# Performance work log

Hardware: AMD Instinct MI355X
Metric: run time of the kernel (lower is better)

The kernel has to match this reference:

```python
import jax, jax.numpy as jnp
import numpy as np

HIDDEN = 512


def lstm_layer(x, W_ih, W_hh, b_ih, b_hh):
    """Single LSTM layer, batch_first. x: [B,T,I] -> hs: [B,T,H].
    PyTorch gate order: i, f, g, o."""
    B = x.shape[0]
    H = W_hh.shape[1]
    # Input contribution for all timesteps at once: [B,T,4H]
    pre = jnp.einsum('bti,gi->btg', x, W_ih) + b_ih + b_hh

    def step(carry, p_t):
        h, c = carry                      # [B,H] each
        gates = p_t + h @ W_hh.T          # [B,4H]
        i, f, g, o = jnp.split(gates, 4, axis=-1)
        i = jax.nn.sigmoid(i)
        f = jax.nn.sigmoid(f)
        g = jnp.tanh(g)
        o = jax.nn.sigmoid(o)
        c = f * c + i * g
        h = o * jnp.tanh(c)
        return (h, c), h

    init = (jnp.zeros((B, H), x.dtype), jnp.zeros((B, H), x.dtype))
    _, hs = jax.lax.scan(step, init, jnp.swapaxes(pre, 0, 1))  # hs: [T,B,H]
    return jnp.swapaxes(hs, 0, 1)


def setup_inputs() -> dict:
    key = jax.random.key(0)
    ks = jax.random.split(key, 11)
    B, T, I, H, C = 128, 512, 64, HIDDEN, 3
    s = 1.0 / np.sqrt(H)  # PyTorch LSTM init scale
    return {
        'state': jax.random.normal(ks[0], (B, T, I), dtype=jnp.float32),
        'W_ih0': jax.random.normal(ks[1], (4 * H, I), dtype=jnp.float32) * s,
        'W_hh0': jax.random.normal(ks[2], (4 * H, H), dtype=jnp.float32) * s,
        'b_ih0': jax.random.normal(ks[3], (4 * H,), dtype=jnp.float32) * s,
        'b_hh0': jax.random.normal(ks[4], (4 * H,), dtype=jnp.float32) * s,
        'W_ih1': jax.random.normal(ks[5], (4 * H, H), dtype=jnp.float32) * s,
        'W_hh1': jax.random.normal(ks[6], (4 * H, H), dtype=jnp.float32) * s,
        'b_ih1': jax.random.normal(ks[7], (4 * H,), dtype=jnp.float32) * s,
        'b_hh1': jax.random.normal(ks[8], (4 * H,), dtype=jnp.float32) * s,
        'W_out': jax.random.normal(ks[9], (C, H), dtype=jnp.float32) * s,
        'b_out': jax.random.normal(ks[10], (C,), dtype=jnp.float32) * s,
    }


def reference(state, W_ih0, W_hh0, b_ih0, b_hh0,
              W_ih1, W_hh1, b_ih1, b_hh1, W_out, b_out):
    # 2-layer LSTM (zero initial h/c, eval mode so inter-layer dropout is inert)
    h1 = lstm_layer(state, W_ih0, W_hh0, b_ih0, b_hh0)  # [B,T,H]
    h2 = lstm_layer(h1, W_ih1, W_hh1, b_ih1, b_hh1)     # [B,T,H]
    last = h2[:, -1, :]                                  # [B,H]
    return last @ W_out.T + b_out                        # [B,nClasses]
```

## Files before the change

kernel.cpp:

```cpp
#include <hip/hip_runtime.h>
#include <hip/hip_bf16.h>
#include <cstddef>

#define B_ 128
#define T_ 512
#define I_ 64
#define H_ 512

typedef __attribute__((ext_vector_type(8))) short short8v;
typedef __attribute__((ext_vector_type(4))) float f32x4;

__device__ __forceinline__ unsigned short f2bf(float f) {
  union { float f; unsigned u; } v; v.f = f;
  unsigned r = (v.u + 0x7FFFu + ((v.u >> 16) & 1u)) >> 16;
  return (unsigned short)r;
}
__device__ __forceinline__ float sigm(float x) { return 1.0f / (1.0f + __expf(-x)); }
__device__ __forceinline__ float tanh_(float x) {
  float t = __expf(2.0f * x);
  return 1.0f - 2.0f / (t + 1.0f);
}

template<int PASS>
__global__ __launch_bounds__(256, 1)
void lstm_pass(const float* __restrict__ Wih, const float* __restrict__ Whh,
               const float* __restrict__ bih, const float* __restrict__ bhh,
               const float* __restrict__ xf32,
               const unsigned short* __restrict__ xbf,
               unsigned int* __restrict__ hhist,
               float* __restrict__ h2last,
               unsigned int* __restrict__ hcomm,
               unsigned int* __restrict__ cnts)
{
  constexpr int KIN = (PASS == 0) ? I_ : H_;
  constexpr int KW  = KIN + H_;
  constexpr int KWS = (PASS == 0) ? 640 : 1024;
  constexpr int NKI = KIN / 32;
  constexpr int NK  = KW / 32;

  __shared__ unsigned short Wl[4 * 16 * KWS];
  __shared__ unsigned short Ah[16 * H_];
  __shared__ float accS[4][16][16];

  const int tid  = threadIdx.x;
  const int wave = tid >> 6;
  const int lane = tid & 63;
  const int lrow = lane & 15;
  const int kgrp = lane >> 4;
  const int g    = blockIdx.x >> 5;
  const int c    = blockIdx.x & 31;
  const int BG0  = g * 16;
  const int HC0  = c * 16;

  for (int idx = tid; idx < 4 * 16 * KW; idx += 256) {
    int k  = idx % KW;
    int rj = idx / KW;
    int jj = rj & 15;
    int w  = rj >> 4;
    int grow = w * H_ + HC0 + jj;
    float wv = (k < KIN) ? Wih[(size_t)grow * KIN + k]
                         : Whh[(size_t)grow * H_ + (k - KIN)];
    int byteoff = ((w * 16 + jj) * KWS + k) * 2;
    byteoff ^= ((jj & 7) << 4);
    *(unsigned short*)((char*)Wl + byteoff) = f2bf(wv);
  }

  const int growB = wave * H_ + HC0 + lrow;
  const float bias = bih[growB] + bhh[growB];

  const int m = tid >> 4;
  const int j = tid & 15;
  float cst = 0.0f;

  unsigned int* cg = cnts + g * 64;

  __syncthreads();

  for (int t = 0; t < T_; ++t) {
    {
      const unsigned long long* src =
          (const unsigned long long*)(hcomm + ((t + 1) & 1) * (B_ * H_ / 2));
      #pragma unroll
      for (int q = 0; q < 8; ++q) {
        unsigned long long v = __hip_atomic_load(
            src + (size_t)(BG0 + m) * (H_ / 4) + j * 8 + q,
            __ATOMIC_RELAXED, __HIP_MEMORY_SCOPE_AGENT);
        int byteoff = (m * H_ + j * 32 + q * 4) * 2;
        byteoff ^= ((m & 7) << 4);
        *(unsigned long long*)((char*)Ah + byteoff) = v;
      }
    }
    __syncthreads();

    f32x4 acc = {0.f, 0.f, 0.f, 0.f};
    #pragma unroll
    for (int kk = 0; kk < NK; ++kk) {
      short8v a, b;
      if (kk < NKI) {
        if (PASS == 0) {
          const float* xp = xf32 + ((size_t)(BG0 + lrow) * T_ + t) * I_ + kk * 32 + kgrp * 8;
          #pragma unroll
          for (int e = 0; e < 8; ++e) a[e] = (short)f2bf(xp[e]);
        } else {
          a = *(const short8v*)(xbf + ((size_t)t * B_ + BG0 + lrow) * H_ + kk * 32 + kgrp * 8);
        }
      } else {
        int byteoff = (lrow * H_ + (kk - NKI) * 32 + kgrp * 8) * 2;
        byteoff ^= ((lrow & 7) << 4);
        a = *(const short8v*)((const char*)Ah + byteoff);
      }
      {
        int byteoff = ((wave * 16 + lrow) * KWS + kk * 32 + kgrp * 8) * 2;
        byteoff ^= ((lrow & 7) << 4);
        b = *(const short8v*)((const char*)Wl + byteoff);
      }
      acc = __builtin_amdgcn_mfma_f32_16x16x32_bf16(a, b, acc, 0, 0, 0);
    }
    #pragma unroll
    for (int r = 0; r < 4; ++r) accS[wave][kgrp * 4 + r][lrow] = acc[r] + bias;
    __syncthreads();

    float xi = accS[0][m][j], xfv = accS[1][m][j], xg = accS[2][m][j], xo = accS[3][m][j];
    float iv = sigm(xi), fv = sigm(xfv), gv = tanh_(xg), ov = sigm(xo);
    cst = fv * cst + iv * gv;
    float hv = ov * tanh_(cst);

    unsigned int hb = f2bf(hv);
    unsigned int ob = ((unsigned int)__shfl_xor((int)hb, 1, 64)) & 0xFFFFu;
    if (!(j & 1)) {
      unsigned int u = (ob << 16) | hb;
      int uidx = ((BG0 + m) * H_ + HC0 + j) >> 1;
      __hip_atomic_store(hcomm + (t & 1) * (B_ * H_ / 2) + uidx, u,
                         __ATOMIC_RELAXED, __HIP_MEMORY_SCOPE_AGENT);
      if (PASS == 0)
        hhist[((size_t)t * B_ + BG0 + m) * (H_ / 2) + ((HC0 + j) >> 1)] = u;
    }
    if (PASS == 1 && t == T_ - 1)
      h2last[(BG0 + m) * H_ + HC0 + j] = hv;

    if (t < T_ - 1) {
      __syncthreads();
      if (tid == 0) {
        __hip_atomic_fetch_add(cg + (c & 3) * 16, 1u,
                               __ATOMIC_RELEASE, __HIP_MEMORY_SCOPE_AGENT);
        const unsigned int target = 32u * (unsigned)(t + 1);
        for (;;) {
          unsigned int s = 0;
          #pragma unroll
          for (int qq = 0; qq < 4; ++qq)
            s += __hip_atomic_load(cg + qq * 16, __ATOMIC_RELAXED, __HIP_MEMORY_SCOPE_AGENT);
          if (s >= target) break;
        }
        __builtin_amdgcn_fence(__ATOMIC_ACQUIRE, "agent");
      }
      __syncthreads();
    }
  }
}

__global__ void out_proj(const float* __restrict__ h2last,
                         const float* __restrict__ Wout,
                         const float* __restrict__ bout,
                         float* __restrict__ out) {
  int o = blockIdx.x;
  int b = o / 3, cc = o - b * 3;
  int ln = threadIdx.x;
  float s = 0.f;
  #pragma unroll
  for (int k = ln; k < H_; k += 64) s += h2last[b * H_ + k] * Wout[cc * H_ + k];
  #pragma unroll
  for (int off = 32; off; off >>= 1) s += __shfl_down(s, off, 64);
  if (ln == 0) out[o] = s + bout[cc];
}

extern "C" void kernel_launch(void* const* d_in, const int* in_sizes, int n_in,
                              void* d_out, int out_size, void* d_ws, size_t ws_size,
                              hipStream_t stream) {
  (void)in_sizes; (void)n_in; (void)out_size; (void)ws_size;
  const float* x    = (const float*)d_in[0];
  const float* Wih0 = (const float*)d_in[1];
  const float* Whh0 = (const float*)d_in[2];
  const float* bih0 = (const float*)d_in[3];
  const float* bhh0 = (const float*)d_in[4];
  const float* Wih1 = (const float*)d_in[5];
  const float* Whh1 = (const float*)d_in[6];
  const float* bih1 = (const float*)d_in[7];
  const float* bhh1 = (const float*)d_in[8];
  const float* Wout = (const float*)d_in[9];
  const float* bout = (const float*)d_in[10];

  char* ws = (char*)d_ws;
  unsigned int* h1ws   = (unsigned int*)(ws);
  float*        h2last = (float*)(ws + 67108864);
  unsigned int* hcommA = (unsigned int*)(ws + 67371008);
  unsigned int* hcommB = (unsigned int*)(ws + 67633152);
  unsigned int* cnts   = (unsigned int*)(ws + 67895296);

  hipMemsetAsync(ws + 67371008, 0, 262144 * 2 + 4096, stream);

  {
    const unsigned short* xbf_null = nullptr;
    float* h2_null = nullptr;
    unsigned int* cA = cnts;
    void* args[10] = {
      (void*)&Wih0, (void*)&Whh0, (void*)&bih0, (void*)&bhh0,
      (void*)&x, (void*)&xbf_null, (void*)&h1ws, (void*)&h2_null,
      (void*)&hcommA, (void*)&cA
    };
    hipLaunchCooperativeKernel(reinterpret_cast<const void*>(&lstm_pass<0>),
                               dim3(256), dim3(256), args, 0, stream);
  }
  {
    const float* xf_null = nullptr;
    const unsigned short* h1bf = (const unsigned short*)h1ws;
    unsigned int* hh_null = nullptr;
    unsigned int* cB = cnts + 512;
    void* args[10] = {
      (void*)&Wih1, (void*)&Whh1, (void*)&bih1, (void*)&bhh1,
      (void*)&xf_null, (void*)&h1bf, (void*)&hh_null, (void*)&h2last,
      (void*)&hcommB, (void*)&cB
    };
    hipLaunchCooperativeKernel(reinterpret_cast<const void*>(&lstm_pass<1>),
                               dim3(256), dim3(256), args, 0, stream);
  }
  out_proj<<<dim3(384), dim3(64), 0, stream>>>(h2last, Wout, bout, (float*)d_out);
}
```

Baseline: 9.165 ms.

## Fuse both LSTM layers into one wavefront-pipelined persistent kernel

Replaces the two sequential cooperative launches with one persistent kernel. Layer 2 runs one timestep behind layer 1, so both layers advance per grid barrier: 513 barrier rounds instead of about 1024. The h1 history buffer in global memory goes away, and the W_ih1 and W_ih0 slices are kept in registers. Gate values are exchanged with lane shuffles instead of a shared-memory staging array. The cost is a wider barrier across 64 blocks per group, each polling 32 counters, plus much higher register pressure from the 16 resident B fragments.

```diff
diff --git a/kernel.cpp b/kernel.cpp
--- a/kernel.cpp
+++ b/kernel.cpp
@@ -21,139 +21,207 @@
   return 1.0f - 2.0f / (t + 1.0f);
 }
 
-template<int PASS>
+__device__ __forceinline__ void cell_update(const f32x4& acc, float bias, int gate,
+                                            float* cst, float* hv) {
+  #pragma unroll
+  for (int r = 0; r < 4; ++r) {
+    float own = acc[r] + bias;
+    float v4  = __shfl_xor(own, 4, 64);
+    float v8  = __shfl_xor(own, 8, 64);
+    float v12 = __shfl_xor(own, 12, 64);
+    float pi = gate==0?own : gate==1?v4 : gate==2?v8  : v12;
+    float pf = gate==1?own : gate==0?v4 : gate==3?v8  : v12;
+    float pg = gate==2?own : gate==3?v4 : gate==0?v8  : v12;
+    float po = gate==3?own : gate==2?v4 : gate==1?v8  : v12;
+    float iv = sigm(pi), fv = sigm(pf), gv = tanh_(pg), ov = sigm(po);
+    cst[r] = fv * cst[r] + iv * gv;
+    hv[r]  = ov * tanh_(cst[r]);
+  }
+}
+
+__device__ __forceinline__ void store_h(const float* hv, unsigned long long* dst,
+                                        int bb, int kgrp, int lane, int u64col) {
+  #pragma unroll
+  for (int r = 0; r < 4; ++r) {
+    unsigned int hb  = f2bf(hv[r]);
+    unsigned int p01 = hb | ((((unsigned)__shfl_xor((int)hb, 1, 64)) & 0xFFFFu) << 16);
+    unsigned int p23 = (unsigned)__shfl_xor((int)p01, 2, 64);
+    if ((lane & 15) == 0) {
+      unsigned long long u = (unsigned long long)p01 | ((unsigned long long)p23 << 32);
+      __hip_atomic_store(dst + (size_t)(bb + kgrp*4 + r) * (H_/4) + u64col, u,
+                         __ATOMIC_RELAXED, __HIP_MEMORY_SCOPE_AGENT);
+    }
+  }
+}
+
 __global__ __launch_bounds__(256, 1)
-void lstm_pass(const float* __restrict__ Wih, const float* __restrict__ Whh,
-               const float* __restrict__ bih, const float* __restrict__ bhh,
-               const float* __restrict__ xf32,
-               const unsigned short* __restrict__ xbf,
-               unsigned int* __restrict__ hhist,
-               float* __restrict__ h2last,
-               unsigned int* __restrict__ hcomm,
-               unsigned int* __restrict__ cnts)
+void lstm_fused(const float* __restrict__ Wih0, const float* __restrict__ Whh0,
+                const float* __restrict__ bih0, const float* __restrict__ bhh0,
+                const float* __restrict__ Wih1, const float* __restrict__ Whh1,
+                const float* __restrict__ bih1, const float* __restrict__ bhh1,
+                const float* __restrict__ x,
+                unsigned long long* __restrict__ hc1,
+                unsigned long long* __restrict__ hc2,
+                float* __restrict__ h2last,
+                unsigned int* __restrict__ cnts)
 {
-  constexpr int KIN = (PASS == 0) ? I_ : H_;
-  constexpr int KW  = KIN + H_;
-  constexpr int KWS = (PASS == 0) ? 640 : 1024;
-  constexpr int NKI = KIN / 32;
-  constexpr int NK  = KW / 32;
-
-  __shared__ unsigned short Wl[4 * 16 * KWS];
-  __shared__ unsigned short Ah[16 * H_];
-  __shared__ float accS[4][16][16];
+  __shared__ unsigned short W0[2*16*512];
+  __shared__ unsigned short W1[2*16*512];
+  __shared__ unsigned short A1[32*512];
+  __shared__ unsigned short A2[32*512];
 
   const int tid  = threadIdx.x;
-  const int wave = tid >> 6;
+  const int w    = tid >> 6;
   const int lane = tid & 63;
-  const int lrow = lane & 15;
+  const int n    = lane & 15;
   const int kgrp = lane >> 4;
-  const int g    = blockIdx.x >> 5;
-  const int c    = blockIdx.x & 31;
-  const int BG0  = g * 16;
-  const int HC0  = c * 16;
-
-  for (int idx = tid; idx < 4 * 16 * KW; idx += 256) {
-    int k  = idx % KW;
-    int rj = idx / KW;
-    int jj = rj & 15;
-    int w  = rj >> 4;
-    int grow = w * H_ + HC0 + jj;
-    float wv = (k < KIN) ? Wih[(size_t)grow * KIN + k]
-                         : Whh[(size_t)grow * H_ + (k - KIN)];
-    int byteoff = ((w * 16 + jj) * KWS + k) * 2;
-    byteoff ^= ((jj & 7) << 4);
-    *(unsigned short*)((char*)Wl + byteoff) = f2bf(wv);
-  }
-
-  const int growB = wave * H_ + HC0 + lrow;
-  const float bias = bih[growB] + bhh[growB];
-
-  const int m = tid >> 4;
-  const int j = tid & 15;
-  float cst = 0.0f;
-
-  unsigned int* cg = cnts + g * 64;
-
-  __syncthreads();
-
-  for (int t = 0; t < T_; ++t) {
+  const int p    = w >> 1;
+  const int mt   = w & 1;
+  const int g    = blockIdx.x >> 6;
+  const int c    = blockIdx.x & 63;
+  const int gate = n >> 2;
+  const int col  = c*8 + p*4 + (n & 3);
+  const int bb   = g*32 + mt*16;
+
+  for (int idx = tid; idx < 2*16*512; idx += 256) {
+    int k  = idx & 511;
+    int rn = idx >> 9;
+    int nn = rn & 15;
+    int pp = rn >> 4;
+    int grow = (nn >> 2)*H_ + c*8 + pp*4 + (nn & 3);
+    int byteoff = (idx*2) ^ ((nn & 7) << 4);
+    *(unsigned short*)((char*)W0 + byteoff) = f2bf(Whh0[(size_t)grow*H_ + k]);
+    *(unsigned short*)((char*)W1 + byteoff) = f2bf(Whh1[(size_t)grow*H_ + k]);
+  }
+
+  short8v breg1[16];
+  #pragma unroll
+  for (int kk = 0; kk < 16; ++kk)
+    #pragma unroll
+    for (int e = 0; e < 8; ++e)
+      breg1[kk][e] = (short)f2bf(Wih1[(size_t)(gate*H_ + col)*H_ + kk*32 + kgrp*8 + e]);
+  short8v bireg0[2];
+  #pragma unroll
+  for (int kk = 0; kk < 2; ++kk)
+    #pragma unroll
+    for (int e = 0; e < 8; ++e)
+      bireg0[kk][e] = (short)f2bf(Wih0[(size_t)(gate*H_ + col)*I_ + kk*32 + kgrp*8 + e]);
+
+  const float bias0 = bih0[gate*H_ + col] + bhh0[gate*H_ + col];
+  const float bias1 = bih1[gate*H_ + col] + bhh1[gate*H_ + col];
+
+  float c1[4] = {0.f,0.f,0.f,0.f}, c2[4] = {0.f,0.f,0.f,0.f};
+
+  const float* xbase = x + (size_t)(bb + n) * T_ * I_;
+  float xr[16];
+  #pragma unroll
+  for (int e = 0; e < 8; ++e) { xr[e] = xbase[kgrp*8 + e]; xr[8+e] = xbase[32 + kgrp*8 + e]; }
+
+  const int srow = tid >> 3;
+  const int t7   = tid & 7;
+  unsigned int* cg = cnts + g*512;
+  const int myline = ((c & 7)*4 + w) * 16;
+  const int aswz  = (n & 7) << 4;
+  const int abase = (mt*16 + n) * 1024;
+  const int bbase = (p*16 + n) * 1024;
+  const int u64col = c*2 + p;
+
+  for (int s = 0; s <= T_; ++s) {
     {
-      const unsigned long long* src =
-          (const unsigned long long*)(hcomm + ((t + 1) & 1) * (B_ * H_ / 2));
-      #pragma unroll
-      for (int q = 0; q < 8; ++q) {
-        unsigned long long v = __hip_atomic_load(
-            src + (size_t)(BG0 + m) * (H_ / 4) + j * 8 + q,
-            __ATOMIC_RELAXED, __HIP_MEMORY_SCOPE_AGENT);
-        int byteoff = (m * H_ + j * 32 + q * 4) * 2;
-        byteoff ^= ((m & 7) << 4);
-        *(unsigned long long*)((char*)Ah + byteoff) = v;
+      const unsigned long long* s1 = hc1 + (size_t)((s+1)&1)*(B_*H_/4) + (size_t)(g*32 + srow)*(H_/4);
+      const unsigned long long* s2 = hc2 + (size_t)(s&1)*(B_*H_/4)     + (size_t)(g*32 + srow)*(H_/4);
+      #pragma unroll
+      for (int ch = 0; ch < 2; ++ch) {
+        unsigned long long tmp[8];
+        #pragma unroll
+        for (int j = 0; j < 8; ++j)
+          tmp[j] = __hip_atomic_load(s1 + (ch*8 + j)*8 + t7, __ATOMIC_RELAXED, __HIP_MEMORY_SCOPE_AGENT);
+        #pragma unroll
+        for (int j = 0; j < 8; ++j) {
+          int q = ch*8 + j;
+          int byteoff = (srow*1024 + (q*8 + t7)*8) ^ ((srow & 7) << 4);
+          *(unsigned long long*)((char*)A1 + byteoff) = tmp[j];
+        }
+      }
+      #pragma unroll
+      for (int ch = 0; ch < 2; ++ch) {
+        unsigned long long tmp[8];
+        #pragma unroll
+        for (int j = 0; j < 8; ++j)
+          tmp[j] = __hip_atomic_load(s2 + (ch*8 + j)*8 + t7, __ATOMIC_RELAXED, __HIP_MEMORY_SCOPE_AGENT);
+        #pragma unroll
+        for (int j = 0; j < 8; ++j) {
+          int q = ch*8 + j;
+          int byteoff = (srow*1024 + (q*8 + t7)*8) ^ ((srow & 7) << 4);
+          *(unsigned long long*)((char*)A2 + byteoff) = tmp[j];
+        }
       }
     }
     __syncthreads();
 
-    f32x4 acc = {0.f, 0.f, 0.f, 0.f};
-    #pragma unroll
-    for (int kk = 0; kk < NK; ++kk) {
-      short8v a, b;
-      if (kk < NKI) {
-        if (PASS == 0) {
-          const float* xp = xf32 + ((size_t)(BG0 + lrow) * T_ + t) * I_ + kk * 32 + kgrp * 8;
+    if (s < T_) {
+      f32x4 acc = {0.f,0.f,0.f,0.f};
+      #pragma unroll
+      for (int kk = 0; kk < 2; ++kk) {
+        short8v a;
+        #pragma unroll
+        for (int e = 0; e < 8; ++e) a[e] = (short)f2bf(xr[kk*8 + e]);
+        acc = __builtin_amdgcn_mfma_f32_16x16x32_bf16(a, bireg0[kk], acc, 0, 0, 0);
+      }
+      #pragma unroll
+      for (int kk = 0; kk < 16; ++kk) {
+        short8v a = *(const short8v*)((const char*)A1 + ((abase + kk*64 + kgrp*16) ^ aswz));
+        short8v b = *(const short8v*)((const char*)W0 + ((bbase + kk*64 + kgrp*16) ^ aswz));
+        acc = __builtin_amdgcn_mfma_f32_16x16x32_bf16(a, b, acc, 0, 0, 0);
+      }
+      float hv[4];
+      cell_update(acc, bias0, gate, c1, hv);
+      store_h(hv, hc1 + (size_t)(s&1)*(B_*H_/4), bb, kgrp, lane, u64col);
+    }
+
+    if (s >= 1) {
+      f32x4 acc = {0.f,0.f,0.f,0.f};
+      #pragma unroll
+      for (int kk = 0; kk < 16; ++kk) {
+        short8v a = *(const short8v*)((const char*)A1 + ((abase + kk*64 + kgrp*16) ^ aswz));
+        acc = __builtin_amdgcn_mfma_f32_16x16x32_bf16(a, breg1[kk], acc, 0, 0, 0);
+      }
+      #pragma unroll
+      for (int kk = 0; kk < 16; ++kk) {
+        short8v a = *(const short8v*)((const char*)A2 + ((abase + kk*64 + kgrp*16) ^ aswz));
+        short8v b = *(const short8v*)((const char*)W1 + ((bbase + kk*64 + kgrp*16) ^ aswz));
+        acc = __builtin_amdgcn_mfma_f32_16x16x32_bf16(a, b, acc, 0, 0, 0);
+      }
+      float hv[4];
+      cell_update(acc, bias1, gate, c2, hv);
+      if (s < T_) {
+        store_h(hv, hc2 + (size_t)((s+1)&1)*(B_*H_/4), bb, kgrp, lane, u64col);
+      } else if (gate == 0) {
+        #pragma unroll
+        for (int r = 0; r < 4; ++r)
+          h2last[(size_t)(bb + kgrp*4 + r)*H_ + col] = hv[r];
+      }
+    }
+
+    if (s + 1 < T_) {
+      const float* xp = xbase + (size_t)(s+1)*I_;
+      #pragma unroll
+      for (int e = 0; e < 8; ++e) { xr[e] = xp[kgrp*8 + e]; xr[8+e] = xp[32 + kgrp*8 + e]; }
+    }
+
+    if (s < T_) {
+      if (lane == 0) {
+        __hip_atomic_fetch_add(cg + myline, 1u, __ATOMIC_RELEASE, __HIP_MEMORY_SCOPE_AGENT);
+        const unsigned target = 256u * (unsigned)(s + 1);
+        for (;;) {
+          unsigned sum = 0;
           #pragma unroll
-          for (int e = 0; e < 8; ++e) a[e] = (short)f2bf(xp[e]);
-        } else {
-          a = *(const short8v*)(xbf + ((size_t)t * B_ + BG0 + lrow) * H_ + kk * 32 + kgrp * 8);
+          for (int qq = 0; qq < 32; ++qq)
+            sum += __hip_atomic_load(cg + qq*16, __ATOMIC_RELAXED, __HIP_MEMORY_SCOPE_AGENT);
+          if (sum >= target) break;
         }
-      } else {
-        int byteoff = (lrow * H_ + (kk - NKI) * 32 + kgrp * 8) * 2;
-        byteoff ^= ((lrow & 7) << 4);
-        a = *(const short8v*)((const char*)Ah + byteoff);
-      }
-      {
-        int byteoff = ((wave * 16 + lrow) * KWS + kk * 32 + kgrp * 8) * 2;
-        byteoff ^= ((lrow & 7) << 4);
-        b = *(const short8v*)((const char*)Wl + byteoff);
-      }
-      acc = __builtin_amdgcn_mfma_f32_16x16x32_bf16(a, b, acc, 0, 0, 0);
-    }
-    #pragma unroll
-    for (int r = 0; r < 4; ++r) accS[wave][kgrp * 4 + r][lrow] = acc[r] + bias;
-    __syncthreads();
-
-    float xi = accS[0][m][j], xfv = accS[1][m][j], xg = accS[2][m][j], xo = accS[3][m][j];
-    float iv = sigm(xi), fv = sigm(xfv), gv = tanh_(xg), ov = sigm(xo);
-    cst = fv * cst + iv * gv;
-    float hv = ov * tanh_(cst);
-
-    unsigned int hb = f2bf(hv);
-    unsigned int ob = ((unsigned int)__shfl_xor((int)hb, 1, 64)) & 0xFFFFu;
-    if (!(j & 1)) {
-      unsigned int u = (ob << 16) | hb;
-      int uidx = ((BG0 + m) * H_ + HC0 + j) >> 1;
-      __hip_atomic_store(hcomm + (t & 1) * (B_ * H_ / 2) + uidx, u,
-                         __ATOMIC_RELAXED, __HIP_MEMORY_SCOPE_AGENT);
-      if (PASS == 0)
-        hhist[((size_t)t * B_ + BG0 + m) * (H_ / 2) + ((HC0 + j) >> 1)] = u;
-    }
-    if (PASS == 1 && t == T_ - 1)
-      h2last[(BG0 + m) * H_ + HC0 + j] = hv;
-
-    if (t < T_ - 1) {
-      __syncthreads();
-      if (tid == 0) {
-        __hip_atomic_fetch_add(cg + (c & 3) * 16, 1u,
-                               __ATOMIC_RELEASE, __HIP_MEMORY_SCOPE_AGENT);
-        const unsigned int target = 32u * (unsigned)(t + 1);
-        for (;;) {
-          unsigned int s = 0;
-          #pragma unroll
-          for (int qq = 0; qq < 4; ++qq)
-            s += __hip_atomic_load(cg + qq * 16, __ATOMIC_RELAXED, __HIP_MEMORY_SCOPE_AGENT);
-          if (s >= target) break;
-        }
-        __builtin_amdgcn_fence(__ATOMIC_ACQUIRE, "agent");
-      }
-      __syncthreads();
+      }
+      __builtin_amdgcn_fence(__ATOMIC_ACQUIRE, "agent");
     }
   }
 }
@@ -190,38 +258,25 @@
   const float* bout = (const float*)d_in[10];
 
   char* ws = (char*)d_ws;
-  unsigned int* h1ws   = (unsigned int*)(ws);
-  float*        h2last = (float*)(ws + 67108864);
-  unsigned int* hcommA = (unsigned int*)(ws + 67371008);
-  unsigned int* hcommB = (unsigned int*)(ws + 67633152);
-  unsigned int* cnts   = (unsigned int*)(ws + 67895296);
-
-  hipMemsetAsync(ws + 67371008, 0, 262144 * 2 + 4096, stream);
-
-  {
-    const unsigned short* xbf_null = nullptr;
-    float* h2_null = nullptr;
-    unsigned int* cA = cnts;
-    void* args[10] = {
-      (void*)&Wih0, (void*)&Whh0, (void*)&bih0, (void*)&bhh0,
-      (void*)&x, (void*)&xbf_null, (void*)&h1ws, (void*)&h2_null,
-      (void*)&hcommA, (void*)&cA
-    };
-    hipLaunchCooperativeKernel(reinterpret_cast<const void*>(&lstm_pass<0>),
-                               dim3(256), dim3(256), args, 0, stream);
-  }
-  {
-    const float* xf_null = nullptr;
-    const unsigned short* h1bf = (const unsigned short*)h1ws;
-    unsigned int* hh_null = nullptr;
-    unsigned int* cB = cnts + 512;
-    void* args[10] = {
-      (void*)&Wih1, (void*)&Whh1, (void*)&bih1, (void*)&bhh1,
-      (void*)&xf_null, (void*)&h1bf, (void*)&hh_null, (void*)&h2last,
-      (void*)&hcommB, (void*)&cB
-    };
-    hipLaunchCooperativeKernel(reinterpret_cast<const void*>(&lstm_pass<1>),
-                               dim3(256), dim3(256), args, 0, stream);
-  }
+  unsigned long long* hc1 = (unsigned long long*)(ws);
+  unsigned long long* hc2 = (unsigned long long*)(ws + 262144);
+  unsigned int* cnts      = (unsigned int*)(ws + 524288);
+  float* h2last           = (float*)(ws + 532480);
+
+  hipMemsetAsync(ws, 0, 532480, stream);
+
+  void* args[12] = {
+    (void*)&Wih0, (void*)&Whh0, (void*)&bih0, (void*)&bhh0,
+    (void*)&Wih1, (void*)&Whh1, (void*)&bih1, (void*)&bhh1,
+    (void*)&x, (void*)&hc1, (void*)&hc2, (void*)&h2last
+  };
+  void* args2[13] = {
+    (void*)&Wih0, (void*)&Whh0, (void*)&bih0, (void*)&bhh0,
+    (void*)&Wih1, (void*)&Whh1, (void*)&bih1, (void*)&bhh1,
+    (void*)&x, (void*)&hc1, (void*)&hc2, (void*)&h2last, (void*)&cnts
+  };
+  (void)args;
+  hipLaunchCooperativeKernel(reinterpret_cast<const void*>(&lstm_fused),
+                             dim3(256), dim3(256), args2, 0, stream);
   out_proj<<<dim3(384), dim3(64), 0, stream>>>(h2last, Wout, bout, (float*)d_out);
 }
```

Result: slower. 14.03 ms (+53.1%).
